# Optimization experiments

Hardware: AMD Instinct MI355X
Metric: run time of the kernel (lower is better)

## Reference

```python
import jax, jax.numpy as jnp
import numpy as np

B, N, T = 512, 24, 25
IN, L, H, OUT = 8, 64, 256, 128


def quat_mul(q, r):
    w1, x1, y1, z1 = jnp.split(q, 4, -1)
    w2, x2, y2, z2 = jnp.split(r, 4, -1)
    return jnp.concatenate([
        w1 * w2 - x1 * x2 - y1 * y2 - z1 * z2,
        w1 * x2 + x1 * w2 + y1 * z2 - z1 * y2,
        w1 * y2 - x1 * z2 + y1 * w2 + z1 * x2,
        w1 * z2 + x1 * y2 - y1 * x2 + z1 * w2], -1)


def node_linear(x, W, b, G):
    # per-node weights [N,F,O], then graph-influence mixing G[N,N]
    y = jnp.einsum('bnf,nfo->bno', x, W) + b
    return jnp.einsum('mn,bno->bmo', G, y)


def graph_linear(x, W, b, G):
    # shared weights [F,O], then graph-influence mixing
    y = jnp.einsum('bnf,fo->bno', x, W) + b
    return jnp.einsum('mn,bno->bmo', G, y)


def lstm_step(x, h, c, Wx, Wh, b, G):
    gates = jnp.einsum('bnf,nfo->bno', x, Wx) + jnp.einsum('bnf,nfo->bno', h, Wh) + b
    gates = jnp.einsum('mn,bno->bmo', G, gates)
    i, f, g, o = jnp.split(gates, 4, -1)
    c = jax.nn.sigmoid(f) * c + jax.nn.sigmoid(i) * jnp.tanh(g)
    h = jax.nn.sigmoid(o) * jnp.tanh(c)
    return h, c


def _p(key, shape, scale):
    return jax.random.normal(key, shape, jnp.float32) * scale


def setup_inputs() -> dict:
    key = jax.random.key(0)
    ks = jax.random.split(key, 20)
    in0 = L + IN
    inp = {
        'x': jax.random.normal(ks[0], (B, 1, N, IN), jnp.float32),
        'enc': jax.random.normal(ks[1], (B, 1, N, H), jnp.float32),
        'z': jax.random.normal(ks[2], (B, 1, N, L), jnp.float32),
        'y': jax.random.normal(ks[3], (B, T, N, 4), jnp.float32),
        'G': jnp.eye(N, dtype=jnp.float32) + 0.02 * jax.random.normal(ks[4], (N, N), jnp.float32),
        'Wx0': _p(ks[5], (N, in0, 4 * OUT), in0 ** -0.5),
        'Wh0': _p(ks[6], (N, OUT, 4 * OUT), OUT ** -0.5),
        'b0': jnp.zeros((N, 4 * OUT), jnp.float32),
        'Wx1': _p(ks[7], (N, OUT, 4 * OUT), OUT ** -0.5),
        'Wh1': _p(ks[8], (N, OUT, 4 * OUT), OUT ** -0.5),
        'b1': jnp.zeros((N, 4 * OUT), jnp.float32),
        'fc_W': _p(ks[9], (N, OUT, OUT), OUT ** -0.5),
        'fc_b': jnp.zeros((N, OUT), jnp.float32),
        'fc2_W': _p(ks[10], (N, OUT, OUT), OUT ** -0.5),
        'fc2_b': jnp.zeros((N, OUT), jnp.float32),
        'ih1_W': _p(ks[11], (H, OUT), H ** -0.5),
        'ih1_b': jnp.zeros((OUT,), jnp.float32),
        'ih2_W': _p(ks[12], (H, OUT), H ** -0.5),
        'ih2_b': jnp.zeros((OUT,), jnp.float32),
        'loc_W': _p(ks[13], (OUT, 3), OUT ** -0.5),
        'loc_b': jnp.zeros((3,), jnp.float32),
        'logz_W': _p(ks[14], (OUT, 4), OUT ** -0.5),
        'logz_b': jnp.zeros((4,), jnp.float32),
    }
    return inp


def reference(x, enc, z, y, G, Wx0, Wh0, b0, Wx1, Wh1, b1, fc_W, fc_b, fc2_W, fc2_b,
              ih1_W, ih1_b, ih2_W, ih2_b, loc_W, loc_b, logz_W, logz_b):
    # eval mode: dropout = identity, no teacher forcing (y unused); rnn2/xi2 are dead code.
    xs, zs, encs = x[:, 0], z[:, 0], enc[:, 0]          # [B,N,*]
    h0 = graph_linear(encs, ih1_W, ih1_b, G)            # shared initial h for both layers
    c0 = graph_linear(encs, ih2_W, ih2_b, G)            # shared initial c for both layers
    loc_start0 = xs[..., :4]
    xi0 = jnp.concatenate([zs, xs], -1)                 # [B,N,L+IN]

    def step(carry, _):
        xi, loc_start, h1, c1, h2, c2 = carry
        h1, c1 = lstm_step(xi, h1, c1, Wx0, Wh0, b0, G)
        h2, c2 = lstm_step(h1, h2, c2, Wx1, Wh1, b1, G)
        yi = jnp.tanh(h2)
        yi1 = jnp.tanh(node_linear(yi, fc_W, fc_b, G))
        yi2 = jnp.tanh(node_linear(yi, fc2_W, fc2_b, G))
        loc3 = graph_linear(yi1, loc_W, loc_b, G)       # [B,N,3]
        log_Z = graph_linear(yi2, logz_W, logz_b, G)    # [B,N,4]
        w = jnp.ones(loc3.shape[:-1] + (1,), loc3.dtype)
        loc4 = jnp.concatenate([w, loc3], -1)
        loc_d = loc4 * jax.lax.rsqrt(jnp.sum(loc4 * loc4, -1, keepdims=True))  # validate
        loc = quat_mul(loc_start, loc_d)                # state_representation.sum
        xi_next = jnp.concatenate([zs, loc, loc_d], -1)
        return (xi_next, loc, h1, c1, h2, c2), (loc, log_Z)

    _, (locs, logzs) = jax.lax.scan(step, (xi0, loc_start0, h0, c0, h0, c0), None, length=T)
    out = jnp.moveaxis(locs, 0, 1)[:, :, None]          # [B,T,1,N,4]
    out_log_diag = jnp.moveaxis(logzs, 0, 1)[:, :, None]
    return out, out_log_diag
```

## Files before the change

### kernel.cpp

```cpp
#include <hip/hip_runtime.h>
#include <math.h>

#define Bsz 512
#define Nn  24
#define Tt  25

typedef _Float16 f16;
typedef _Float16 f16x8 __attribute__((ext_vector_type(8)));
typedef float f32x4 __attribute__((ext_vector_type(4)));

template <int FM, int FN>
__global__ __launch_bounds__(256) void gemm_mfma(
    const f16* __restrict__ A16, const float* __restrict__ A32, int Ka,
    const f16* __restrict__ W, size_t wstride,
    const float* __restrict__ bias, int bstride,
    float* __restrict__ Y, int O)
{
    const int BM = FM * 32, BN = FN * 32;
    const int n  = blockIdx.z;
    const int b0 = blockIdx.y * BM;
    const int o0 = blockIdx.x * BN;
    const int tid  = threadIdx.x;
    const int wave = tid >> 6, lane = tid & 63;
    const int wm = (wave >> 1) * FM * 16;
    const int wn = (wave & 1) * FN * 16;
    const int m16 = lane & 15, quad = lane >> 4;

    __shared__ __attribute__((aligned(16))) f16 sA[BM][72];
    __shared__ __attribute__((aligned(16))) f16 sW[BN][72];

    const f16* Wn = W + (size_t)n * wstride;
    f32x4 acc[FM][FN] = {};

    const int r  = tid >> 3;
    const int cc = (tid & 7) * 8;

    for (int k0 = 0; k0 < Ka; k0 += 64) {
        if (A16) {
            for (int row = r; row < BM; row += 32) {
                const f16x8* src = (const f16x8*)&A16[((size_t)(b0 + row) * Nn + n) * Ka + k0 + cc];
                *(f16x8*)&sA[row][cc] = *src;
            }
        } else {
            for (int row = r; row < BM; row += 32) {
                const float* src = &A32[((size_t)(b0 + row) * Nn + n) * Ka + k0 + cc];
                f16x8 v;
#pragma unroll
                for (int u = 0; u < 8; u++) v[u] = (f16)src[u];
                *(f16x8*)&sA[row][cc] = v;
            }
        }
        for (int row = r; row < BN; row += 32) {
            const f16x8* src = (const f16x8*)&Wn[(size_t)(o0 + row) * Ka + k0 + cc];
            *(f16x8*)&sW[row][cc] = *src;
        }
        __syncthreads();
#pragma unroll
        for (int kk = 0; kk < 64; kk += 32) {
            f16x8 af[FM], bf[FN];
#pragma unroll
            for (int i = 0; i < FM; i++)
                af[i] = *(const f16x8*)&sA[wm + i * 16 + m16][kk + quad * 8];
#pragma unroll
            for (int j = 0; j < FN; j++)
                bf[j] = *(const f16x8*)&sW[wn + j * 16 + m16][kk + quad * 8];
#pragma unroll
            for (int i = 0; i < FM; i++)
#pragma unroll
                for (int j = 0; j < FN; j++)
                    acc[i][j] = __builtin_amdgcn_mfma_f32_16x16x32_f16(af[i], bf[j], acc[i][j], 0, 0, 0);
        }
        __syncthreads();
    }
#pragma unroll
    for (int i = 0; i < FM; i++) {
#pragma unroll
        for (int j = 0; j < FN; j++) {
            int ocol = o0 + wn + j * 16 + m16;
            float bv = bias[(size_t)n * bstride + ocol];
#pragma unroll
            for (int rg = 0; rg < 4; rg++) {
                int brow = b0 + wm + i * 16 + quad * 4 + rg;
                Y[((size_t)brow * Nn + n) * O + ocol] = acc[i][j][rg] + bv;
            }
        }
    }
}

__global__ __launch_bounds__(256) void prep_w01(
    const float* __restrict__ Wx0, const float* __restrict__ Wh0,
    const float* __restrict__ Wx1, const float* __restrict__ Wh1,
    f16* __restrict__ Wt0, f16* __restrict__ Wt1)
{
    size_t idx = (size_t)blockIdx.x * 256 + threadIdx.x;
    const size_t total = (size_t)Nn * 512 * 256;
    if (idx >= total) return;
    int k = idx & 255;
    size_t no = idx >> 8;
    int o = no & 511;
    int n = (int)(no >> 9);
    float v0 = 0.f;
    if (k < 72) v0 = Wx0[((size_t)n * 72 + k) * 512 + o];
    else if (k < 200) v0 = Wh0[((size_t)n * 128 + (k - 72)) * 512 + o];
    Wt0[idx] = (f16)v0;
    float v1 = (k < 128) ? Wx1[((size_t)n * 128 + k) * 512 + o]
                         : Wh1[((size_t)n * 128 + (k - 128)) * 512 + o];
    Wt1[idx] = (f16)v1;
}

__global__ __launch_bounds__(256) void prep_wf(
    const float* __restrict__ fcW, const float* __restrict__ fc2W,
    f16* __restrict__ Wtf)
{
    size_t idx = (size_t)blockIdx.x * 256 + threadIdx.x;
    const size_t total = (size_t)Nn * 256 * 128;
    if (idx >= total) return;
    int k = idx & 127;
    size_t no = idx >> 7;
    int o = no & 255;
    int n = (int)(no >> 8);
    float v = (o < 128) ? fcW[((size_t)n * 128 + k) * 128 + o]
                        : fc2W[((size_t)n * 128 + k) * 128 + (o - 128)];
    Wtf[idx] = (f16)v;
}

__global__ __launch_bounds__(256) void prep_wi(
    const float* __restrict__ ih1W, const float* __restrict__ ih2W,
    const float* __restrict__ ih1b, const float* __restrict__ ih2b,
    const float* __restrict__ fcb, const float* __restrict__ fc2b,
    f16* __restrict__ Wti, float* __restrict__ bi, float* __restrict__ bcat)
{
    int idx = blockIdx.x * 256 + threadIdx.x;
    int k = idx & 255, o = idx >> 8;
    Wti[idx] = (f16)((o < 128) ? ih1W[(size_t)k * 128 + o] : ih2W[(size_t)k * 128 + (o - 128)]);
    if (idx < 256) bi[idx] = (idx < 128) ? ih1b[idx] : ih2b[idx - 128];
    if (idx < Nn * 256) {
        int n = idx >> 8, oo = idx & 255;
        bcat[idx] = (oo < 128) ? fcb[n * 128 + oo] : fc2b[n * 128 + (oo - 128)];
    }
}

__global__ __launch_bounds__(256) void init_xi(
    const float* __restrict__ x, const float* __restrict__ z,
    f16* __restrict__ xi, float* __restrict__ ls)
{
    size_t idx = (size_t)blockIdx.x * 256 + threadIdx.x;
    const size_t total = (size_t)Bsz * Nn * 256;
    if (idx < total) {
        size_t bn = idx >> 8;
        int k = idx & 255;
        if (k < 64) xi[idx] = (f16)z[bn * 64 + k];
        else if (k < 72) xi[idx] = (f16)x[bn * 8 + (k - 64)];
        else if (k >= 200) xi[idx] = (f16)0.f;
    }
    if (idx < (size_t)Bsz * Nn * 4) {
        size_t bn = idx >> 2;
        int j = idx & 3;
        ls[idx] = x[bn * 8 + j];
    }
}

__global__ __launch_bounds__(256) void mix_init(
    const float* __restrict__ Yhc, const float* __restrict__ G,
    f16* __restrict__ xi_cat, f16* __restrict__ l2cat,
    float* __restrict__ c1, float* __restrict__ c2)
{
    const int b = blockIdx.x;
    const int tid = threadIdx.x;
    __shared__ float sY[6144], sG[576];
    for (int i = tid; i < 576; i += 256) sG[i] = G[i];
    for (int i = tid; i < 6144; i += 256) sY[i] = Yhc[(size_t)b * 6144 + i];
    __syncthreads();
    for (int w = tid; w < 3072; w += 256) {
        int o = w & 127, m = w >> 7;
        float ah = 0.f, ac = 0.f;
#pragma unroll
        for (int n = 0; n < 24; n++) {
            float g = sG[m * 24 + n];
            ah += g * sY[n * 256 + o];
            ac += g * sY[n * 256 + 128 + o];
        }
        size_t row = (size_t)b * 24 + m;
        f16 hf = (f16)ah;
        xi_cat[row * 256 + 72 + o] = hf;
        l2cat[row * 256 + o] = hf;
        l2cat[row * 256 + 128 + o] = hf;
        c1[row * 128 + o] = ac;
        c2[row * 128 + o] = ac;
    }
}

__global__ __launch_bounds__(256) void mixlstm(
    const float* __restrict__ Ypre, const float* __restrict__ G,
    float* __restrict__ c,
    f16* __restrict__ dstA, int strideA,
    f16* __restrict__ dstB, int strideB, int tanhB)
{
    const int b = blockIdx.x;
    const int jt = blockIdx.y * 64;
    const int tid = threadIdx.x;
    __shared__ float sY[24 * 4 * 64];
    __shared__ float sG[576];
    for (int i = tid; i < 576; i += 256) sG[i] = G[i];
    for (int i = tid; i < 6144; i += 256) {
        int j = i & 63, g = (i >> 6) & 3, n = i >> 8;
        sY[i] = Ypre[((size_t)b * 24 + n) * 512 + g * 128 + jt + j];
    }
    __syncthreads();
    for (int w = tid; w < 1536; w += 256) {
        int j = w & 63, m = w >> 6;
        float gi = 0.f, gf = 0.f, gg = 0.f, go = 0.f;
        const float* gr = &sG[m * 24];
#pragma unroll
        for (int n = 0; n < 24; n++) {
            float g = gr[n];
            gi += g * sY[n * 256 + j];
            gf += g * sY[n * 256 + 64 + j];
            gg += g * sY[n * 256 + 128 + j];
            go += g * sY[n * 256 + 192 + j];
        }
        int col = jt + j;
        size_t row = (size_t)b * 24 + m;
        float cv = c[row * 128 + col];
        float si = 1.f / (1.f + expf(-gi));
        float sf = 1.f / (1.f + expf(-gf));
        float so = 1.f / (1.f + expf(-go));
        float tg = tanhf(gg);
        cv = sf * cv + si * tg;
        c[row * 128 + col] = cv;
        float h = so * tanhf(cv);
        dstA[row * strideA + col] = (f16)h;
        dstB[row * strideB + col] = (f16)(tanhB ? tanhf(h) : h);
    }
}

__global__ __launch_bounds__(256) void finstep(
    const float* __restrict__ p, const float* __restrict__ G,
    const float* __restrict__ locW, const float* __restrict__ locb,
    const float* __restrict__ lzW, const float* __restrict__ lzb,
    float* __restrict__ ls, f16* __restrict__ xi,
    float* __restrict__ out, int t)
{
    const int b = blockIdx.x;
    const int tid = threadIdx.x;
    __shared__ float sP[6144], sY1[3072], sY2[3072];
    __shared__ float sG[576];
    __shared__ float sLp[24][3], sZp[24][4], sL3[24][3], sZ3[24][4];
    for (int i = tid; i < 576; i += 256) sG[i] = G[i];
    for (int i = tid; i < 6144; i += 256) sP[i] = p[(size_t)b * 6144 + i];
    __syncthreads();
    for (int w = tid; w < 3072; w += 256) {
        int o = w & 127, m = w >> 7;
        float a1 = 0.f, a2 = 0.f;
#pragma unroll
        for (int n = 0; n < 24; n++) {
            float g = sG[m * 24 + n];
            a1 += g * sP[n * 256 + o];
            a2 += g * sP[n * 256 + 128 + o];
        }
        sY1[w] = tanhf(a1);
        sY2[w] = tanhf(a2);
    }
    __syncthreads();
    if (tid < 72) {
        int m = tid / 3, j = tid - m * 3;
        float s = locb[j];
        for (int o = 0; o < 128; o++) s += sY1[m * 128 + o] * locW[o * 3 + j];
        sLp[m][j] = s;
    } else if (tid < 168) {
        int w2 = tid - 72; int m = w2 >> 2, j = w2 & 3;
        float s = lzb[j];
        for (int o = 0; o < 128; o++) s += sY2[m * 128 + o] * lzW[o * 4 + j];
        sZp[m][j] = s;
    }
    __syncthreads();
    if (tid < 72) {
        int m = tid / 3, j = tid - m * 3;
        float s = 0.f;
#pragma unroll
        for (int n = 0; n < 24; n++) s += sG[m * 24 + n] * sLp[n][j];
        sL3[m][j] = s;
    } else if (tid < 168) {
        int w2 = tid - 72; int m = w2 >> 2, j = w2 & 3;
        float s = 0.f;
#pragma unroll
        for (int n = 0; n < 24; n++) s += sG[m * 24 + n] * sZp[n][j];
        sZ3[m][j] = s;
    }
    __syncthreads();
    if (tid < 24) {
        int m = tid;
        float xx = sL3[m][0], xy = sL3[m][1], xz = sL3[m][2];
        float r = rsqrtf(1.f + xx * xx + xy * xy + xz * xz);
        float dw = r, dx = xx * r, dy = xy * r, dz = xz * r;
        size_t li = ((size_t)b * 24 + m) * 4;
        float qw = ls[li], qx = ls[li + 1], qy = ls[li + 2], qz = ls[li + 3];
        float lw = qw * dw - qx * dx - qy * dy - qz * dz;
        float lx = qw * dx + qx * dw + qy * dz - qz * dy;
        float ly = qw * dy - qx * dz + qy * dw + qz * dx;
        float lz = qw * dz + qx * dy - qy * dx + qz * dw;
        size_t oi = (((size_t)b * Tt + t) * Nn + m) * 4;
        out[oi + 0] = lw; out[oi + 1] = lx; out[oi + 2] = ly; out[oi + 3] = lz;
        size_t zi = (size_t)Bsz * Tt * Nn * 4 + oi;
        out[zi + 0] = sZ3[m][0]; out[zi + 1] = sZ3[m][1];
        out[zi + 2] = sZ3[m][2]; out[zi + 3] = sZ3[m][3];
        ls[li] = lw; ls[li + 1] = lx; ls[li + 2] = ly; ls[li + 3] = lz;
        size_t xb = ((size_t)b * 24 + m) * 256 + 64;
        xi[xb + 0] = (f16)lw; xi[xb + 1] = (f16)lx; xi[xb + 2] = (f16)ly; xi[xb + 3] = (f16)lz;
        xi[xb + 4] = (f16)dw; xi[xb + 5] = (f16)dx; xi[xb + 6] = (f16)dy; xi[xb + 7] = (f16)dz;
    }
}

extern "C" void kernel_launch(void* const* d_in, const int* in_sizes, int n_in,
                              void* d_out, int out_size, void* d_ws, size_t ws_size,
                              hipStream_t stream)
{
    const float* x    = (const float*)d_in[0];
    const float* enc  = (const float*)d_in[1];
    const float* z    = (const float*)d_in[2];
    const float* G    = (const float*)d_in[4];
    const float* Wx0  = (const float*)d_in[5];
    const float* Wh0  = (const float*)d_in[6];
    const float* b0   = (const float*)d_in[7];
    const float* Wx1  = (const float*)d_in[8];
    const float* Wh1  = (const float*)d_in[9];
    const float* b1   = (const float*)d_in[10];
    const float* fcW  = (const float*)d_in[11];
    const float* fcb  = (const float*)d_in[12];
    const float* fc2W = (const float*)d_in[13];
    const float* fc2b = (const float*)d_in[14];
    const float* ih1W = (const float*)d_in[15];
    const float* ih1b = (const float*)d_in[16];
    const float* ih2W = (const float*)d_in[17];
    const float* ih2b = (const float*)d_in[18];
    const float* locW = (const float*)d_in[19];
    const float* locb = (const float*)d_in[20];
    const float* lzW  = (const float*)d_in[21];
    const float* lzb  = (const float*)d_in[22];
    float* out = (float*)d_out;

    const size_t BN = (size_t)Bsz * Nn;
    char* wp = (char*)d_ws;
    size_t off = 0;
    auto carve = [&](size_t bytes) -> char* {
        char* pc = wp + off;
        off += (bytes + 255) & ~(size_t)255;
        return pc;
    };
    f16*   Wt0    = (f16*)carve((size_t)Nn * 512 * 256 * 2);
    f16*   Wt1    = (f16*)carve((size_t)Nn * 512 * 256 * 2);
    f16*   Wtf    = (f16*)carve((size_t)Nn * 256 * 128 * 2);
    f16*   Wti    = (f16*)carve((size_t)256 * 256 * 2);
    float* bcat   = (float*)carve((size_t)Nn * 256 * 4);
    float* bi     = (float*)carve(256 * 4);
    f16*   xi_cat = (f16*)carve(BN * 256 * 2);
    f16*   l2cat  = (f16*)carve(BN * 256 * 2);
    f16*   yib    = (f16*)carve(BN * 128 * 2);
    float* c1     = (float*)carve(BN * 128 * 4);
    float* c2     = (float*)carve(BN * 128 * 4);
    float* ls     = (float*)carve(BN * 4 * 4);
    float* yp     = (float*)carve(BN * 512 * 4);

    prep_w01<<<(int)(((size_t)Nn * 512 * 256 + 255) / 256), 256, 0, stream>>>(Wx0, Wh0, Wx1, Wh1, Wt0, Wt1);
    prep_wf<<<(int)(((size_t)Nn * 256 * 128 + 255) / 256), 256, 0, stream>>>(fcW, fc2W, Wtf);
    prep_wi<<<256, 256, 0, stream>>>(ih1W, ih2W, ih1b, ih2b, fcb, fc2b, Wti, bi, bcat);
    init_xi<<<(int)((BN * 256 + 255) / 256), 256, 0, stream>>>(x, z, xi_cat, ls);

    gemm_mfma<2, 2><<<dim3(4, 8, 24), 256, 0, stream>>>(
        nullptr, enc, 256, Wti, 0, bi, 0, yp, 256);
    mix_init<<<512, 256, 0, stream>>>(yp, G, xi_cat, l2cat, c1, c2);

    for (int t = 0; t < Tt; t++) {
        gemm_mfma<2, 4><<<dim3(4, 8, 24), 256, 0, stream>>>(
            xi_cat, nullptr, 256, Wt0, (size_t)512 * 256, b0, 512, yp, 512);
        mixlstm<<<dim3(512, 2), 256, 0, stream>>>(yp, G, c1, xi_cat + 72, 256, l2cat, 256, 0);
        gemm_mfma<2, 4><<<dim3(4, 8, 24), 256, 0, stream>>>(
            l2cat, nullptr, 256, Wt1, (size_t)512 * 256, b1, 512, yp, 512);
        mixlstm<<<dim3(512, 2), 256, 0, stream>>>(yp, G, c2, l2cat + 128, 256, yib, 128, 1);
        gemm_mfma<2, 2><<<dim3(4, 8, 24), 256, 0, stream>>>(
            yib, nullptr, 128, Wtf, (size_t)256 * 128, bcat, 256, yp, 256);
        finstep<<<512, 256, 0, stream>>>(yp, G, locW, locb, lzW, lzb, ls, xi_cat, out, t);
    }
}
```

Measured before the change: 2.486 ms.

## Hoist constant z-projection out of recurrence and store gate pre-activations in fp16

The z part of the layer-0 input is the same at every step. Its projection (plus bias) is now computed once into a base buffer, which is added in the GEMM epilogue, and the recurrent K shrinks from 256 to 192. GEMM outputs are written as fp16 instead of fp32 with transposed tiling (weights as the M operand, vectorized 4-wide stores), halving the intermediate traffic read by the mixing kernels. This costs extra fp16 rounding on the pre-activations and an extra base-buffer read each step.

```diff
diff --git a/kernel.cpp b/kernel.cpp
--- a/kernel.cpp
+++ b/kernel.cpp
@@ -7,27 +7,29 @@
 
 typedef _Float16 f16;
 typedef _Float16 f16x8 __attribute__((ext_vector_type(8)));
+typedef _Float16 f16x4 __attribute__((ext_vector_type(4)));
 typedef float f32x4 __attribute__((ext_vector_type(4)));
 
 template <int FM, int FN>
 __global__ __launch_bounds__(256) void gemm_mfma(
-    const f16* __restrict__ A16, const float* __restrict__ A32, int Ka,
+    const f16* __restrict__ Act, const float* __restrict__ Act32, int Ka,
     const f16* __restrict__ W, size_t wstride,
     const float* __restrict__ bias, int bstride,
-    float* __restrict__ Y, int O)
+    const f16* __restrict__ base16,
+    f16* __restrict__ Y, int O)
 {
     const int BM = FM * 32, BN = FN * 32;
     const int n  = blockIdx.z;
-    const int b0 = blockIdx.y * BM;
-    const int o0 = blockIdx.x * BN;
+    const int o0 = blockIdx.x * BM;
+    const int b0 = blockIdx.y * BN;
     const int tid  = threadIdx.x;
     const int wave = tid >> 6, lane = tid & 63;
     const int wm = (wave >> 1) * FM * 16;
     const int wn = (wave & 1) * FN * 16;
     const int m16 = lane & 15, quad = lane >> 4;
 
-    __shared__ __attribute__((aligned(16))) f16 sA[BM][72];
-    __shared__ __attribute__((aligned(16))) f16 sW[BN][72];
+    __shared__ __attribute__((aligned(16))) f16 sW[BM][72];
+    __shared__ __attribute__((aligned(16))) f16 sB[BN][72];
 
     const f16* Wn = W + (size_t)n * wstride;
     f32x4 acc[FM][FN] = {};
@@ -36,23 +38,19 @@
     const int cc = (tid & 7) * 8;
 
     for (int k0 = 0; k0 < Ka; k0 += 64) {
-        if (A16) {
-            for (int row = r; row < BM; row += 32) {
-                const f16x8* src = (const f16x8*)&A16[((size_t)(b0 + row) * Nn + n) * Ka + k0 + cc];
-                *(f16x8*)&sA[row][cc] = *src;
+        for (int row = r; row < BM; row += 32)
+            *(f16x8*)&sW[row][cc] = *(const f16x8*)&Wn[(size_t)(o0 + row) * Ka + k0 + cc];
+        if (Act) {
+            for (int row = r; row < BN; row += 32)
+                *(f16x8*)&sB[row][cc] = *(const f16x8*)&Act[((size_t)(b0 + row) * Nn + n) * Ka + k0 + cc];
+        } else {
+            for (int row = r; row < BN; row += 32) {
+                const float* src = &Act32[((size_t)(b0 + row) * Nn + n) * Ka + k0 + cc];
+                f16x8 v;
+#pragma unroll
+                for (int u = 0; u < 8; u++) v[u] = (f16)src[u];
+                *(f16x8*)&sB[row][cc] = v;
             }
-        } else {
-            for (int row = r; row < BM; row += 32) {
-                const float* src = &A32[((size_t)(b0 + row) * Nn + n) * Ka + k0 + cc];
-                f16x8 v;
-#pragma unroll
-                for (int u = 0; u < 8; u++) v[u] = (f16)src[u];
-                *(f16x8*)&sA[row][cc] = v;
-            }
-        }
-        for (int row = r; row < BN; row += 32) {
-            const f16x8* src = (const f16x8*)&Wn[(size_t)(o0 + row) * Ka + k0 + cc];
-            *(f16x8*)&sW[row][cc] = *src;
         }
         __syncthreads();
 #pragma unroll
@@ -60,10 +58,10 @@
             f16x8 af[FM], bf[FN];
 #pragma unroll
             for (int i = 0; i < FM; i++)
-                af[i] = *(const f16x8*)&sA[wm + i * 16 + m16][kk + quad * 8];
+                af[i] = *(const f16x8*)&sW[wm + i * 16 + m16][kk + quad * 8];
 #pragma unroll
             for (int j = 0; j < FN; j++)
-                bf[j] = *(const f16x8*)&sW[wn + j * 16 + m16][kk + quad * 8];
+                bf[j] = *(const f16x8*)&sB[wn + j * 16 + m16][kk + quad * 8];
 #pragma unroll
             for (int i = 0; i < FM; i++)
 #pragma unroll
@@ -74,15 +72,24 @@
     }
 #pragma unroll
     for (int i = 0; i < FM; i++) {
+        const int orow = o0 + wm + i * 16 + quad * 4;
+        float4 bv = make_float4(0.f, 0.f, 0.f, 0.f);
+        if (bias) bv = *(const float4*)&bias[(size_t)n * bstride + orow];
 #pragma unroll
         for (int j = 0; j < FN; j++) {
-            int ocol = o0 + wn + j * 16 + m16;
-            float bv = bias[(size_t)n * bstride + ocol];
-#pragma unroll
-            for (int rg = 0; rg < 4; rg++) {
-                int brow = b0 + wm + i * 16 + quad * 4 + rg;
-                Y[((size_t)brow * Nn + n) * O + ocol] = acc[i][j][rg] + bv;
+            const int bcol = b0 + wn + j * 16 + m16;
+            size_t yi = ((size_t)bcol * Nn + n) * (size_t)O + orow;
+            float v0 = acc[i][j][0] + bv.x;
+            float v1 = acc[i][j][1] + bv.y;
+            float v2 = acc[i][j][2] + bv.z;
+            float v3 = acc[i][j][3] + bv.w;
+            if (base16) {
+                f16x4 bb = *(const f16x4*)&base16[yi];
+                v0 += (float)bb[0]; v1 += (float)bb[1];
+                v2 += (float)bb[2]; v3 += (float)bb[3];
             }
+            f16x4 o4; o4[0] = (f16)v0; o4[1] = (f16)v1; o4[2] = (f16)v2; o4[3] = (f16)v3;
+            *(f16x4*)&Y[yi] = o4;
         }
     }
 }
@@ -90,22 +97,33 @@
 __global__ __launch_bounds__(256) void prep_w01(
     const float* __restrict__ Wx0, const float* __restrict__ Wh0,
     const float* __restrict__ Wx1, const float* __restrict__ Wh1,
-    f16* __restrict__ Wt0, f16* __restrict__ Wt1)
+    f16* __restrict__ Wz, f16* __restrict__ Wt0, f16* __restrict__ Wt1)
 {
     size_t idx = (size_t)blockIdx.x * 256 + threadIdx.x;
-    const size_t total = (size_t)Nn * 512 * 256;
-    if (idx >= total) return;
-    int k = idx & 255;
-    size_t no = idx >> 8;
-    int o = no & 511;
-    int n = (int)(no >> 9);
-    float v0 = 0.f;
-    if (k < 72) v0 = Wx0[((size_t)n * 72 + k) * 512 + o];
-    else if (k < 200) v0 = Wh0[((size_t)n * 128 + (k - 72)) * 512 + o];
-    Wt0[idx] = (f16)v0;
-    float v1 = (k < 128) ? Wx1[((size_t)n * 128 + k) * 512 + o]
-                         : Wh1[((size_t)n * 128 + (k - 128)) * 512 + o];
-    Wt1[idx] = (f16)v1;
+    const size_t nz = (size_t)Nn * 512 * 64;
+    const size_t n0 = (size_t)Nn * 512 * 192;
+    const size_t n1 = (size_t)Nn * 512 * 256;
+    if (idx < nz) {
+        int k = idx & 63; int o = (idx >> 6) & 511; int n = (int)(idx >> 15);
+        Wz[idx] = (f16)Wx0[((size_t)n * 72 + k) * 512 + o];
+    } else if (idx < nz + n0) {
+        size_t i2 = idx - nz;
+        int k = (int)(i2 % 192);
+        size_t no = i2 / 192;
+        int o = (int)(no & 511); int n = (int)(no >> 9);
+        float v = 0.f;
+        if (k < 8) v = Wx0[((size_t)n * 72 + 64 + k) * 512 + o];
+        else if (k < 136) v = Wh0[((size_t)n * 128 + (k - 8)) * 512 + o];
+        Wt0[i2] = (f16)v;
+    } else if (idx < nz + n0 + n1) {
+        size_t i3 = idx - nz - n0;
+        int k = (int)(i3 & 255);
+        size_t no = i3 >> 8;
+        int o = (int)(no & 511); int n = (int)(no >> 9);
+        float v = (k < 128) ? Wx1[((size_t)n * 128 + k) * 512 + o]
+                            : Wh1[((size_t)n * 128 + (k - 128)) * 512 + o];
+        Wt1[i3] = (f16)v;
+    }
 }
 
 __global__ __launch_bounds__(256) void prep_wf(
@@ -113,12 +131,10 @@
     f16* __restrict__ Wtf)
 {
     size_t idx = (size_t)blockIdx.x * 256 + threadIdx.x;
-    const size_t total = (size_t)Nn * 256 * 128;
-    if (idx >= total) return;
-    int k = idx & 127;
+    if (idx >= (size_t)Nn * 256 * 128) return;
+    int k = (int)(idx & 127);
     size_t no = idx >> 7;
-    int o = no & 255;
-    int n = (int)(no >> 8);
+    int o = (int)(no & 255); int n = (int)(no >> 8);
     float v = (o < 128) ? fcW[((size_t)n * 128 + k) * 128 + o]
                         : fc2W[((size_t)n * 128 + k) * 128 + (o - 128)];
     Wtf[idx] = (f16)v;
@@ -141,35 +157,38 @@
 }
 
 __global__ __launch_bounds__(256) void init_xi(
-    const float* __restrict__ x, const float* __restrict__ z,
-    f16* __restrict__ xi, float* __restrict__ ls)
+    const float* __restrict__ x, f16* __restrict__ xi2, float* __restrict__ ls)
 {
     size_t idx = (size_t)blockIdx.x * 256 + threadIdx.x;
-    const size_t total = (size_t)Bsz * Nn * 256;
+    const size_t total = (size_t)Bsz * Nn * 192;
     if (idx < total) {
-        size_t bn = idx >> 8;
-        int k = idx & 255;
-        if (k < 64) xi[idx] = (f16)z[bn * 64 + k];
-        else if (k < 72) xi[idx] = (f16)x[bn * 8 + (k - 64)];
-        else if (k >= 200) xi[idx] = (f16)0.f;
+        size_t bn = idx / 192;
+        int k = (int)(idx - bn * 192);
+        if (k < 8) xi2[idx] = (f16)x[bn * 8 + k];
+        else if (k >= 136) xi2[idx] = (f16)0.f;
     }
     if (idx < (size_t)Bsz * Nn * 4) {
         size_t bn = idx >> 2;
-        int j = idx & 3;
-        ls[idx] = x[bn * 8 + j];
+        ls[idx] = x[bn * 8 + (idx & 3)];
     }
 }
 
 __global__ __launch_bounds__(256) void mix_init(
-    const float* __restrict__ Yhc, const float* __restrict__ G,
-    f16* __restrict__ xi_cat, f16* __restrict__ l2cat,
+    const f16* __restrict__ Yhc, const float* __restrict__ G,
+    f16* __restrict__ xi2, f16* __restrict__ l2cat,
     float* __restrict__ c1, float* __restrict__ c2)
 {
     const int b = blockIdx.x;
     const int tid = threadIdx.x;
     __shared__ float sY[6144], sG[576];
     for (int i = tid; i < 576; i += 256) sG[i] = G[i];
-    for (int i = tid; i < 6144; i += 256) sY[i] = Yhc[(size_t)b * 6144 + i];
+    for (int v = tid; v < 768; v += 256) {
+        int c8 = (v & 31) * 8, n = v >> 5;
+        f16x8 t = *(const f16x8*)&Yhc[((size_t)b * Nn + n) * 256 + c8];
+        float* d = &sY[n * 256 + c8];
+#pragma unroll
+        for (int u = 0; u < 8; u++) d[u] = (float)t[u];
+    }
     __syncthreads();
     for (int w = tid; w < 3072; w += 256) {
         int o = w & 127, m = w >> 7;
@@ -180,9 +199,9 @@
             ah += g * sY[n * 256 + o];
             ac += g * sY[n * 256 + 128 + o];
         }
-        size_t row = (size_t)b * 24 + m;
+        size_t row = (size_t)b * Nn + m;
         f16 hf = (f16)ah;
-        xi_cat[row * 256 + 72 + o] = hf;
+        xi2[row * 192 + 8 + o] = hf;
         l2cat[row * 256 + o] = hf;
         l2cat[row * 256 + 128 + o] = hf;
         c1[row * 128 + o] = ac;
@@ -191,7 +210,7 @@
 }
 
 __global__ __launch_bounds__(256) void mixlstm(
-    const float* __restrict__ Ypre, const float* __restrict__ G,
+    const f16* __restrict__ Ypre, const float* __restrict__ G,
     float* __restrict__ c,
     f16* __restrict__ dstA, int strideA,
     f16* __restrict__ dstB, int strideB, int tanhB)
@@ -199,12 +218,15 @@
     const int b = blockIdx.x;
     const int jt = blockIdx.y * 64;
     const int tid = threadIdx.x;
-    __shared__ float sY[24 * 4 * 64];
+    __shared__ float sY[6144];
     __shared__ float sG[576];
     for (int i = tid; i < 576; i += 256) sG[i] = G[i];
-    for (int i = tid; i < 6144; i += 256) {
-        int j = i & 63, g = (i >> 6) & 3, n = i >> 8;
-        sY[i] = Ypre[((size_t)b * 24 + n) * 512 + g * 128 + jt + j];
+    for (int v = tid; v < 768; v += 256) {
+        int j8 = (v & 7) * 8, g = (v >> 3) & 3, n = v >> 5;
+        f16x8 t = *(const f16x8*)&Ypre[((size_t)b * Nn + n) * 512 + g * 128 + jt + j8];
+        float* d = &sY[n * 256 + g * 64 + j8];
+#pragma unroll
+        for (int u = 0; u < 8; u++) d[u] = (float)t[u];
     }
     __syncthreads();
     for (int w = tid; w < 1536; w += 256) {
@@ -220,7 +242,7 @@
             go += g * sY[n * 256 + 192 + j];
         }
         int col = jt + j;
-        size_t row = (size_t)b * 24 + m;
+        size_t row = (size_t)b * Nn + m;
         float cv = c[row * 128 + col];
         float si = 1.f / (1.f + expf(-gi));
         float sf = 1.f / (1.f + expf(-gf));
@@ -235,10 +257,10 @@
 }
 
 __global__ __launch_bounds__(256) void finstep(
-    const float* __restrict__ p, const float* __restrict__ G,
+    const f16* __restrict__ p, const float* __restrict__ G,
     const float* __restrict__ locW, const float* __restrict__ locb,
     const float* __restrict__ lzW, const float* __restrict__ lzb,
-    float* __restrict__ ls, f16* __restrict__ xi,
+    float* __restrict__ ls, f16* __restrict__ xi2,
     float* __restrict__ out, int t)
 {
     const int b = blockIdx.x;
@@ -247,7 +269,13 @@
     __shared__ float sG[576];
     __shared__ float sLp[24][3], sZp[24][4], sL3[24][3], sZ3[24][4];
     for (int i = tid; i < 576; i += 256) sG[i] = G[i];
-    for (int i = tid; i < 6144; i += 256) sP[i] = p[(size_t)b * 6144 + i];
+    for (int v = tid; v < 768; v += 256) {
+        int c8 = (v & 31) * 8, n = v >> 5;
+        f16x8 tv = *(const f16x8*)&p[((size_t)b * Nn + n) * 256 + c8];
+        float* d = &sP[n * 256 + c8];
+#pragma unroll
+        for (int u = 0; u < 8; u++) d[u] = (float)tv[u];
+    }
     __syncthreads();
     for (int w = tid; w < 3072; w += 256) {
         int o = w & 127, m = w >> 7;
@@ -293,7 +321,7 @@
         float xx = sL3[m][0], xy = sL3[m][1], xz = sL3[m][2];
         float r = rsqrtf(1.f + xx * xx + xy * xy + xz * xz);
         float dw = r, dx = xx * r, dy = xy * r, dz = xz * r;
-        size_t li = ((size_t)b * 24 + m) * 4;
+        size_t li = ((size_t)b * Nn + m) * 4;
         float qw = ls[li], qx = ls[li + 1], qy = ls[li + 2], qz = ls[li + 3];
         float lw = qw * dw - qx * dx - qy * dy - qz * dz;
         float lx = qw * dx + qx * dw + qy * dz - qz * dy;
@@ -305,9 +333,9 @@
         out[zi + 0] = sZ3[m][0]; out[zi + 1] = sZ3[m][1];
         out[zi + 2] = sZ3[m][2]; out[zi + 3] = sZ3[m][3];
         ls[li] = lw; ls[li + 1] = lx; ls[li + 2] = ly; ls[li + 3] = lz;
-        size_t xb = ((size_t)b * 24 + m) * 256 + 64;
-        xi[xb + 0] = (f16)lw; xi[xb + 1] = (f16)lx; xi[xb + 2] = (f16)ly; xi[xb + 3] = (f16)lz;
-        xi[xb + 4] = (f16)dw; xi[xb + 5] = (f16)dx; xi[xb + 6] = (f16)dy; xi[xb + 7] = (f16)dz;
+        size_t xb = ((size_t)b * Nn + m) * 192;
+        xi2[xb + 0] = (f16)lw; xi2[xb + 1] = (f16)lx; xi2[xb + 2] = (f16)ly; xi2[xb + 3] = (f16)lz;
+        xi2[xb + 4] = (f16)dw; xi2[xb + 5] = (f16)dx; xi2[xb + 6] = (f16)dy; xi2[xb + 7] = (f16)dz;
     }
 }
 
@@ -321,10 +349,10 @@
     const float* G    = (const float*)d_in[4];
     const float* Wx0  = (const float*)d_in[5];
     const float* Wh0  = (const float*)d_in[6];
-    const float* b0   = (const float*)d_in[7];
+    const float* b0i  = (const float*)d_in[7];
     const float* Wx1  = (const float*)d_in[8];
     const float* Wh1  = (const float*)d_in[9];
-    const float* b1   = (const float*)d_in[10];
+    const float* b1i  = (const float*)d_in[10];
     const float* fcW  = (const float*)d_in[11];
     const float* fcb  = (const float*)d_in[12];
     const float* fc2W = (const float*)d_in[13];
@@ -347,38 +375,43 @@
         off += (bytes + 255) & ~(size_t)255;
         return pc;
     };
-    f16*   Wt0    = (f16*)carve((size_t)Nn * 512 * 256 * 2);
+    f16*   Wz     = (f16*)carve((size_t)Nn * 512 * 64 * 2);
+    f16*   Wt0    = (f16*)carve((size_t)Nn * 512 * 192 * 2);
     f16*   Wt1    = (f16*)carve((size_t)Nn * 512 * 256 * 2);
     f16*   Wtf    = (f16*)carve((size_t)Nn * 256 * 128 * 2);
     f16*   Wti    = (f16*)carve((size_t)256 * 256 * 2);
     float* bcat   = (float*)carve((size_t)Nn * 256 * 4);
     float* bi     = (float*)carve(256 * 4);
-    f16*   xi_cat = (f16*)carve(BN * 256 * 2);
+    f16*   base1  = (f16*)carve(BN * 512 * 2);
+    f16*   xi2    = (f16*)carve(BN * 192 * 2);
     f16*   l2cat  = (f16*)carve(BN * 256 * 2);
     f16*   yib    = (f16*)carve(BN * 128 * 2);
     float* c1     = (float*)carve(BN * 128 * 4);
     float* c2     = (float*)carve(BN * 128 * 4);
     float* ls     = (float*)carve(BN * 4 * 4);
-    float* yp     = (float*)carve(BN * 512 * 4);
-
-    prep_w01<<<(int)(((size_t)Nn * 512 * 256 + 255) / 256), 256, 0, stream>>>(Wx0, Wh0, Wx1, Wh1, Wt0, Wt1);
-    prep_wf<<<(int)(((size_t)Nn * 256 * 128 + 255) / 256), 256, 0, stream>>>(fcW, fc2W, Wtf);
+    f16*   yp     = (f16*)carve(BN * 512 * 2);
+    f16*   pbuf   = (f16*)carve(BN * 256 * 2);
+
+    prep_w01<<<24576, 256, 0, stream>>>(Wx0, Wh0, Wx1, Wh1, Wz, Wt0, Wt1);
+    prep_wf<<<3072, 256, 0, stream>>>(fcW, fc2W, Wtf);
     prep_wi<<<256, 256, 0, stream>>>(ih1W, ih2W, ih1b, ih2b, fcb, fc2b, Wti, bi, bcat);
-    init_xi<<<(int)((BN * 256 + 255) / 256), 256, 0, stream>>>(x, z, xi_cat, ls);
-
-    gemm_mfma<2, 2><<<dim3(4, 8, 24), 256, 0, stream>>>(
-        nullptr, enc, 256, Wti, 0, bi, 0, yp, 256);
-    mix_init<<<512, 256, 0, stream>>>(yp, G, xi_cat, l2cat, c1, c2);
+    init_xi<<<9216, 256, 0, stream>>>(x, xi2, ls);
+
+    gemm_mfma<2, 4><<<dim3(8, 4, 24), 256, 0, stream>>>(
+        nullptr, z, 64, Wz, (size_t)512 * 64, b0i, 512, nullptr, base1, 512);
+    gemm_mfma<2, 4><<<dim3(4, 4, 24), 256, 0, stream>>>(
+        nullptr, enc, 256, Wti, 0, bi, 0, nullptr, yp, 256);
+    mix_init<<<512, 256, 0, stream>>>(yp, G, xi2, l2cat, c1, c2);
 
     for (int t = 0; t < Tt; t++) {
-        gemm_mfma<2, 4><<<dim3(4, 8, 24), 256, 0, stream>>>(
-            xi_cat, nullptr, 256, Wt0, (size_t)512 * 256, b0, 512, yp, 512);
-        mixlstm<<<dim3(512, 2), 256, 0, stream>>>(yp, G, c1, xi_cat + 72, 256, l2cat, 256, 0);
-        gemm_mfma<2, 4><<<dim3(4, 8, 24), 256, 0, stream>>>(
-            l2cat, nullptr, 256, Wt1, (size_t)512 * 256, b1, 512, yp, 512);
+        gemm_mfma<2, 4><<<dim3(8, 4, 24), 256, 0, stream>>>(
+            xi2, nullptr, 192, Wt0, (size_t)512 * 192, nullptr, 0, base1, yp, 512);
+        mixlstm<<<dim3(512, 2), 256, 0, stream>>>(yp, G, c1, xi2 + 8, 192, l2cat, 256, 0);
+        gemm_mfma<2, 4><<<dim3(8, 4, 24), 256, 0, stream>>>(
+            l2cat, nullptr, 256, Wt1, (size_t)512 * 256, b1i, 512, nullptr, yp, 512);
         mixlstm<<<dim3(512, 2), 256, 0, stream>>>(yp, G, c2, l2cat + 128, 256, yib, 128, 1);
-        gemm_mfma<2, 2><<<dim3(4, 8, 24), 256, 0, stream>>>(
-            yib, nullptr, 128, Wtf, (size_t)256 * 128, bcat, 256, yp, 256);
-        finstep<<<512, 256, 0, stream>>>(yp, G, locW, locb, lzW, lzb, ls, xi_cat, out, t);
-    }
-}
+        gemm_mfma<2, 4><<<dim3(4, 4, 24), 256, 0, stream>>>(
+            yib, nullptr, 128, Wtf, (size_t)256 * 128, bcat, 256, nullptr, pbuf, 256);
+        finstep<<<512, 256, 0, stream>>>(pbuf, G, locW, locb, lzW, lzb, ls, xi2, out, t);
+    }
+}
```

Result: no change. 2.479 ms (-0.3%).
